# Performance work log

Hardware: AMD Instinct MI355X
Metric: run time of the kernel (lower is better)

## Reference

```python
import jax, jax.numpy as jnp
import numpy as np
from jax import lax

B, C, H, W = 256, 768, 24, 24


def _corner_mask(h, w):
    # corners are never considered peaks in the original nested loops
    m = np.zeros((h, w), dtype=bool)
    m[[0, 0, -1, -1], [0, -1, 0, -1]] = True
    return jnp.asarray(m)


def get_peaks_pool(feat):
    # feat: [B, C, H, W]
    hm = jnp.mean(feat, axis=1)  # [B, H, W]
    # 3x3 local max/min with window clipped at the image border (SAME pad with
    # identity elements), exactly matching the original edge-case loops.
    mx = lax.reduce_window(hm, -jnp.inf, lax.max, (1, 3, 3), (1, 1, 1), 'SAME')
    mn = lax.reduce_window(hm, jnp.inf, lax.min, (1, 3, 3), (1, 1, 1), 'SAME')
    corner = _corner_mask(hm.shape[1], hm.shape[2])
    max_mask = ((hm >= mx) & ~corner).astype(feat.dtype)  # [B, H, W]
    min_mask = ((hm <= mn) & ~corner).astype(feat.dtype)
    # masked mean of feature vectors at peak locations
    f_max = jnp.einsum('bchw,bhw->bc', feat, max_mask) / jnp.sum(max_mask, axis=(1, 2))[:, None]
    f_min = jnp.einsum('bchw,bhw->bc', feat, min_mask) / jnp.sum(min_mask, axis=(1, 2))[:, None]
    f_gap = jnp.mean(feat, axis=(2, 3))  # global average pool
    return jnp.stack([f_max, f_min, f_gap], axis=2)  # [B, C, 3]


def _l2norm(x):
    return x / jnp.linalg.norm(x, axis=-1, keepdims=True)


def _cross_entropy(logits):
    # labels = arange(B): mean of -log_softmax diagonal
    logp = jax.nn.log_softmax(logits, axis=-1)
    return -jnp.mean(jnp.diagonal(logp))


def setup_inputs() -> dict:
    key = jax.random.key(0)
    k1, k2 = jax.random.split(key)
    return {
        'image_features1': jax.random.normal(k1, (B, C, H, W), dtype=jnp.float32),
        'image_features2': jax.random.normal(k2, (B, C, H, W), dtype=jnp.float32),
        'logit_scale': jnp.full((1,), 14.285, dtype=jnp.float32),
    }


def reference(image_features1, image_features2, logit_scale):
    p1 = get_peaks_pool(image_features1)  # [B, C, 3]
    p2 = get_peaks_pool(image_features2)
    e1 = _l2norm(jnp.concatenate([p1[:, :, 0], p1[:, :, 1], p1[:, :, 2]], axis=-1))  # [B, 3C]
    e2 = _l2norm(jnp.concatenate([p2[:, :, 0], p2[:, :, 1], p2[:, :, 2]], axis=-1))
    logits1 = logit_scale.reshape(()) * (e1 @ e2.T)  # [B, B]
    logits2 = logits1.T
    return (_cross_entropy(logits1) + _cross_entropy(logits2)) / 2
```

## Files before the change

kernel.cpp:

```cpp
#include <hip/hip_runtime.h>
#include <math.h>

#define BB   256
#define CC   768
#define HHX  24
#define WWX  24
#define HWX  576
#define EDIM 2304
#define NIMG 2

__global__ void k1_hm(const float* __restrict__ f1, const float* __restrict__ f2,
                      float* __restrict__ hm) {
    int blk = blockIdx.x;
    int img = blk >> 8;
    int b   = blk & 255;
    const float* base = ((img == 0) ? f1 : f2) + (size_t)b * CC * HWX;
    int t = threadIdx.x;
    float acc = 0.f;
    #pragma unroll 8
    for (int c = 0; c < CC; ++c)
        acc += base[(size_t)c * HWX + t];
    hm[(size_t)blk * HWX + t] = acc;
}

__global__ void k2_mask(const float* __restrict__ hm, float* __restrict__ mmax,
                        float* __restrict__ mmin, float* __restrict__ cnt) {
    int blk = blockIdx.x;
    int t = threadIdx.x;
    __shared__ float sh[HWX];
    __shared__ int c0, c1;
    if (t == 0) { c0 = 0; c1 = 0; }
    float v = hm[(size_t)blk * HWX + t];
    sh[t] = v;
    __syncthreads();

    int h = t / WWX, w = t % WWX;
    float mx = -__builtin_inff(), mn = __builtin_inff();
    #pragma unroll
    for (int dh = -1; dh <= 1; ++dh) {
        int hh = h + dh;
        if (hh < 0 || hh >= HHX) continue;
        #pragma unroll
        for (int dw = -1; dw <= 1; ++dw) {
            int ww = w + dw;
            if (ww < 0 || ww >= WWX) continue;
            float u = sh[hh * WWX + ww];
            mx = fmaxf(mx, u);
            mn = fminf(mn, u);
        }
    }
    bool corner = (t == 0) || (t == WWX - 1) || (t == (HHX - 1) * WWX) || (t == HWX - 1);
    bool ismax = (v >= mx) && !corner;
    bool ismin = (v <= mn) && !corner;
    mmax[(size_t)blk * HWX + t] = ismax ? 1.f : 0.f;
    mmin[(size_t)blk * HWX + t] = ismin ? 1.f : 0.f;
    if (ismax) atomicAdd(&c0, 1);
    if (ismin) atomicAdd(&c1, 1);
    __syncthreads();
    if (t == 0) {
        cnt[blk * 2 + 0] = (float)c0;
        cnt[blk * 2 + 1] = (float)c1;
    }
}

__global__ void k3_sums(const float* __restrict__ f1, const float* __restrict__ f2,
                        const float* __restrict__ mmax, const float* __restrict__ mmin,
                        float* __restrict__ sums) {
    int blk = blockIdx.x;
    int img = blk >> 8, b = blk & 255;
    const float* base = ((img == 0) ? f1 : f2) + (size_t)b * CC * HWX;
    int lane = threadIdx.x & 63;
    int wv   = threadIdx.x >> 6;

    float mm[9], mn[9];
    #pragma unroll
    for (int j = 0; j < 9; ++j) {
        mm[j] = mmax[(size_t)blk * HWX + lane + 64 * j];
        mn[j] = mmin[(size_t)blk * HWX + lane + 64 * j];
    }
    float* out = sums + (size_t)blk * EDIM;

    for (int c = wv; c < CC; c += 4) {
        const float* p = base + (size_t)c * HWX;
        float s0 = 0.f, s1 = 0.f, s2 = 0.f;
        #pragma unroll
        for (int j = 0; j < 9; ++j) {
            float v = p[lane + 64 * j];
            s0 += v;
            s1 = fmaf(v, mm[j], s1);
            s2 = fmaf(v, mn[j], s2);
        }
        #pragma unroll
        for (int off = 32; off; off >>= 1) {
            s0 += __shfl_down(s0, off, 64);
            s1 += __shfl_down(s1, off, 64);
            s2 += __shfl_down(s2, off, 64);
        }
        if (lane == 0) {
            out[c]          = s1;
            out[CC + c]     = s2;
            out[2 * CC + c] = s0;
        }
    }
}

__global__ void k4_norm(float* __restrict__ sums, const float* __restrict__ cnt,
                        float* __restrict__ e2t) {
    int blk = blockIdx.x;
    int img = blk >> 8, b = blk & 255;
    int t = threadIdx.x;
    float invmax = 1.f / cnt[blk * 2 + 0];
    float invmin = 1.f / cnt[blk * 2 + 1];
    const float invgap = 1.f / (float)HWX;
    float* e = sums + (size_t)blk * EDIM;

    float val[9];
    float sq = 0.f;
    #pragma unroll
    for (int j = 0; j < 9; ++j) {
        int k = t + 256 * j;
        float d = (k < CC) ? invmax : (k < 2 * CC) ? invmin : invgap;
        float v = e[k] * d;
        val[j] = v;
        sq = fmaf(v, v, sq);
    }
    __shared__ float red[256];
    red[t] = sq;
    __syncthreads();
    for (int s = 128; s; s >>= 1) {
        if (t < s) red[t] += red[t + s];
        __syncthreads();
    }
    float rn = 1.f / sqrtf(red[0]);
    #pragma unroll
    for (int j = 0; j < 9; ++j) {
        int k = t + 256 * j;
        float v = val[j] * rn;
        e[k] = v;
        if (img == 1) e2t[(size_t)k * BB + b] = v;
    }
}

__global__ void k5_logits(const float* __restrict__ e, const float* __restrict__ e2t,
                          const float* __restrict__ scale_p, float* __restrict__ logits) {
    int blk = blockIdx.x;
    int j = threadIdx.x;
    __shared__ float s1[4][EDIM];
    for (int r = 0; r < 4; ++r)
        for (int k = j; k < EDIM; k += 256)
            s1[r][k] = e[(size_t)(4 * blk + r) * EDIM + k];
    __syncthreads();
    float scale = scale_p[0];
    float a0 = 0.f, a1 = 0.f, a2 = 0.f, a3 = 0.f;
    for (int k = 0; k < EDIM; ++k) {
        float bv = e2t[(size_t)k * BB + j];
        a0 = fmaf(s1[0][k], bv, a0);
        a1 = fmaf(s1[1][k], bv, a1);
        a2 = fmaf(s1[2][k], bv, a2);
        a3 = fmaf(s1[3][k], bv, a3);
    }
    logits[(size_t)(4 * blk + 0) * BB + j] = scale * a0;
    logits[(size_t)(4 * blk + 1) * BB + j] = scale * a1;
    logits[(size_t)(4 * blk + 2) * BB + j] = scale * a2;
    logits[(size_t)(4 * blk + 3) * BB + j] = scale * a3;
}

__global__ void k6_loss(const float* __restrict__ logits, float* __restrict__ out) {
    int i = threadIdx.x;
    float rmax = -__builtin_inff(), cmax = -__builtin_inff();
    for (int k = 0; k < BB; ++k) {
        rmax = fmaxf(rmax, logits[(size_t)i * BB + k]);
        cmax = fmaxf(cmax, logits[(size_t)k * BB + i]);
    }
    float rs = 0.f, cs = 0.f;
    for (int k = 0; k < BB; ++k) {
        rs += expf(logits[(size_t)i * BB + k] - rmax);
        cs += expf(logits[(size_t)k * BB + i] - cmax);
    }
    float lser = rmax + logf(rs);
    float lsec = cmax + logf(cs);
    float diag = logits[(size_t)i * BB + i];
    float v = 0.5f * (lser + lsec) - diag;

    __shared__ float red[256];
    red[i] = v;
    __syncthreads();
    for (int s = 128; s; s >>= 1) {
        if (i < s) red[i] += red[i + s];
        __syncthreads();
    }
    if (i == 0) out[0] = red[0] * (1.f / (float)BB);
}

extern "C" void kernel_launch(void* const* d_in, const int* in_sizes, int n_in,
                              void* d_out, int out_size, void* d_ws, size_t ws_size,
                              hipStream_t stream) {
    const float* f1 = (const float*)d_in[0];
    const float* f2 = (const float*)d_in[1];
    const float* scale_p = (const float*)d_in[2];
    float* out = (float*)d_out;

    float* ws = (float*)d_ws;
    const size_t off_hm     = 0;
    const size_t off_mmax   = off_hm     + (size_t)NIMG * BB * HWX;
    const size_t off_mmin   = off_mmax   + (size_t)NIMG * BB * HWX;
    const size_t off_cnt    = off_mmin   + (size_t)NIMG * BB * HWX;
    const size_t off_sums   = off_cnt    + (size_t)NIMG * BB * 2;
    const size_t off_e2t    = off_sums   + (size_t)NIMG * BB * EDIM;
    const size_t off_logits = off_e2t    + (size_t)EDIM * BB;

    float* hm     = ws + off_hm;
    float* mmax   = ws + off_mmax;
    float* mmin   = ws + off_mmin;
    float* cnt    = ws + off_cnt;
    float* sums   = ws + off_sums;
    float* e2t    = ws + off_e2t;
    float* logits = ws + off_logits;

    hipLaunchKernelGGL(k1_hm,    dim3(NIMG * BB), dim3(HWX), 0, stream, f1, f2, hm);
    hipLaunchKernelGGL(k2_mask,  dim3(NIMG * BB), dim3(HWX), 0, stream, hm, mmax, mmin, cnt);
    hipLaunchKernelGGL(k3_sums,  dim3(NIMG * BB), dim3(256), 0, stream, f1, f2, mmax, mmin, sums);
    hipLaunchKernelGGL(k4_norm,  dim3(NIMG * BB), dim3(256), 0, stream, sums, cnt, e2t);
    hipLaunchKernelGGL(k5_logits, dim3(64),       dim3(256), 0, stream, sums, e2t, scale_p, logits);
    hipLaunchKernelGGL(k6_loss,  dim3(1),         dim3(256), 0, stream, logits, out);
}
```

Before: 1.207 ms.

## Vectorize feature reads, fuse mask into sums kernel, parallelize logits and loss

The channel-sum kernel now reads float4 and splits channels across four thread groups with a shared-memory final reduction. The mask computation moves into the weighted-sum kernel, keeping masks in shared memory, and that kernel uses 512 threads with float4 loads. The logits kernel now computes two rows per block and also writes a transposed copy. The single-block loss is split into a parallel row/column log-sum-exp kernel plus a small final reduction. The intent is to raise memory bandwidth on the two full passes over the features and to remove the serial loss loop, at the cost of more kernels and extra workspace.

```diff
diff --git a/kernel.cpp b/kernel.cpp
--- a/kernel.cpp
+++ b/kernel.cpp
@@ -6,6 +6,7 @@
 #define HHX  24
 #define WWX  24
 #define HWX  576
+#define HW4  144
 #define EDIM 2304
 #define NIMG 2
 
@@ -15,81 +16,106 @@
     int img = blk >> 8;
     int b   = blk & 255;
     const float* base = ((img == 0) ? f1 : f2) + (size_t)b * CC * HWX;
+    const float4* base4 = (const float4*)base;
     int t = threadIdx.x;
-    float acc = 0.f;
+    int pos4 = t % HW4;
+    int cg   = t / HW4;
+    float4 acc = make_float4(0.f, 0.f, 0.f, 0.f);
     #pragma unroll 8
-    for (int c = 0; c < CC; ++c)
-        acc += base[(size_t)c * HWX + t];
-    hm[(size_t)blk * HWX + t] = acc;
-}
-
-__global__ void k2_mask(const float* __restrict__ hm, float* __restrict__ mmax,
-                        float* __restrict__ mmin, float* __restrict__ cnt) {
-    int blk = blockIdx.x;
+    for (int c = cg; c < CC; c += 4) {
+        float4 v = base4[(size_t)c * HW4 + pos4];
+        acc.x += v.x; acc.y += v.y; acc.z += v.z; acc.w += v.w;
+    }
+    __shared__ float4 part[HWX];
+    part[t] = acc;
+    __syncthreads();
+    if (t < HW4) {
+        float4 a = part[t], b4 = part[t + HW4], c4 = part[t + 2 * HW4], d4 = part[t + 3 * HW4];
+        float4 s;
+        s.x = a.x + b4.x + c4.x + d4.x;
+        s.y = a.y + b4.y + c4.y + d4.y;
+        s.z = a.z + b4.z + c4.z + d4.z;
+        s.w = a.w + b4.w + c4.w + d4.w;
+        ((float4*)(hm + (size_t)blk * HWX))[t] = s;
+    }
+}
+
+__global__ void k3_sums(const float* __restrict__ f1, const float* __restrict__ f2,
+                        const float* __restrict__ hm, float* __restrict__ cnt,
+                        float* __restrict__ sums) {
+    int blk = blockIdx.x;
+    int img = blk >> 8, b = blk & 255;
+    const float* base = ((img == 0) ? f1 : f2) + (size_t)b * CC * HWX;
     int t = threadIdx.x;
-    __shared__ float sh[HWX];
+    int lane = t & 63;
+    int wv   = t >> 6;
+
+    __shared__ __align__(16) float sh[HWX];
+    __shared__ __align__(16) float smm[HWX];
+    __shared__ __align__(16) float smn[HWX];
     __shared__ int c0, c1;
+
+    sh[t] = hm[(size_t)blk * HWX + t];
+    if (t < HWX - 512) sh[512 + t] = hm[(size_t)blk * HWX + 512 + t];
     if (t == 0) { c0 = 0; c1 = 0; }
-    float v = hm[(size_t)blk * HWX + t];
-    sh[t] = v;
-    __syncthreads();
-
-    int h = t / WWX, w = t % WWX;
-    float mx = -__builtin_inff(), mn = __builtin_inff();
-    #pragma unroll
-    for (int dh = -1; dh <= 1; ++dh) {
-        int hh = h + dh;
-        if (hh < 0 || hh >= HHX) continue;
+    __syncthreads();
+
+    for (int p = t; p < HWX; p += 512) {
+        int h = p / WWX, w = p % WWX;
+        float v = sh[p];
+        float mx = -__builtin_inff(), mn = __builtin_inff();
         #pragma unroll
-        for (int dw = -1; dw <= 1; ++dw) {
-            int ww = w + dw;
-            if (ww < 0 || ww >= WWX) continue;
-            float u = sh[hh * WWX + ww];
-            mx = fmaxf(mx, u);
-            mn = fminf(mn, u);
+        for (int dh = -1; dh <= 1; ++dh) {
+            int hh = h + dh;
+            if (hh < 0 || hh >= HHX) continue;
+            #pragma unroll
+            for (int dw = -1; dw <= 1; ++dw) {
+                int ww = w + dw;
+                if (ww < 0 || ww >= WWX) continue;
+                float u = sh[hh * WWX + ww];
+                mx = fmaxf(mx, u);
+                mn = fminf(mn, u);
+            }
         }
-    }
-    bool corner = (t == 0) || (t == WWX - 1) || (t == (HHX - 1) * WWX) || (t == HWX - 1);
-    bool ismax = (v >= mx) && !corner;
-    bool ismin = (v <= mn) && !corner;
-    mmax[(size_t)blk * HWX + t] = ismax ? 1.f : 0.f;
-    mmin[(size_t)blk * HWX + t] = ismin ? 1.f : 0.f;
-    if (ismax) atomicAdd(&c0, 1);
-    if (ismin) atomicAdd(&c1, 1);
+        bool corner = (p == 0) || (p == WWX - 1) || (p == (HHX - 1) * WWX) || (p == HWX - 1);
+        bool ismax = (v >= mx) && !corner;
+        bool ismin = (v <= mn) && !corner;
+        smm[p] = ismax ? 1.f : 0.f;
+        smn[p] = ismin ? 1.f : 0.f;
+        if (ismax) atomicAdd(&c0, 1);
+        if (ismin) atomicAdd(&c1, 1);
+    }
     __syncthreads();
     if (t == 0) {
         cnt[blk * 2 + 0] = (float)c0;
         cnt[blk * 2 + 1] = (float)c1;
     }
-}
-
-__global__ void k3_sums(const float* __restrict__ f1, const float* __restrict__ f2,
-                        const float* __restrict__ mmax, const float* __restrict__ mmin,
-                        float* __restrict__ sums) {
-    int blk = blockIdx.x;
-    int img = blk >> 8, b = blk & 255;
-    const float* base = ((img == 0) ? f1 : f2) + (size_t)b * CC * HWX;
-    int lane = threadIdx.x & 63;
-    int wv   = threadIdx.x >> 6;
-
-    float mm[9], mn[9];
-    #pragma unroll
-    for (int j = 0; j < 9; ++j) {
-        mm[j] = mmax[(size_t)blk * HWX + lane + 64 * j];
-        mn[j] = mmin[(size_t)blk * HWX + lane + 64 * j];
-    }
+
+    float4 ma0 = ((const float4*)smm)[lane];
+    float4 ma1 = ((const float4*)smm)[64 + lane];
+    float  ma2 = smm[512 + lane];
+    float4 mi0 = ((const float4*)smn)[lane];
+    float4 mi1 = ((const float4*)smn)[64 + lane];
+    float  mi2 = smn[512 + lane];
+
     float* out = sums + (size_t)blk * EDIM;
 
-    for (int c = wv; c < CC; c += 4) {
-        const float* p = base + (size_t)c * HWX;
-        float s0 = 0.f, s1 = 0.f, s2 = 0.f;
-        #pragma unroll
-        for (int j = 0; j < 9; ++j) {
-            float v = p[lane + 64 * j];
-            s0 += v;
-            s1 = fmaf(v, mm[j], s1);
-            s2 = fmaf(v, mn[j], s2);
-        }
+    for (int c = wv; c < CC; c += 8) {
+        const float4* p4 = (const float4*)(base + (size_t)c * HWX);
+        float4 v0 = p4[lane];
+        float4 v1 = p4[64 + lane];
+        float  v2 = (base + (size_t)c * HWX)[512 + lane];
+
+        float s0 = v0.x + v0.y + v0.z + v0.w + v1.x + v1.y + v1.z + v1.w + v2;
+        float s1 = v0.x * ma0.x + v0.y * ma0.y + v0.z * ma0.z + v0.w * ma0.w;
+        s1 = fmaf(v1.x, ma1.x, s1); s1 = fmaf(v1.y, ma1.y, s1);
+        s1 = fmaf(v1.z, ma1.z, s1); s1 = fmaf(v1.w, ma1.w, s1);
+        s1 = fmaf(v2, ma2, s1);
+        float s2 = v0.x * mi0.x + v0.y * mi0.y + v0.z * mi0.z + v0.w * mi0.w;
+        s2 = fmaf(v1.x, mi1.x, s2); s2 = fmaf(v1.y, mi1.y, s2);
+        s2 = fmaf(v1.z, mi1.z, s2); s2 = fmaf(v1.w, mi1.w, s2);
+        s2 = fmaf(v2, mi2, s2);
+
         #pragma unroll
         for (int off = 32; off; off >>= 1) {
             s0 += __shfl_down(s0, off, 64);
@@ -142,46 +168,54 @@
 }
 
 __global__ void k5_logits(const float* __restrict__ e, const float* __restrict__ e2t,
-                          const float* __restrict__ scale_p, float* __restrict__ logits) {
+                          const float* __restrict__ scale_p, float* __restrict__ logits,
+                          float* __restrict__ logitsT) {
     int blk = blockIdx.x;
     int j = threadIdx.x;
-    __shared__ float s1[4][EDIM];
-    for (int r = 0; r < 4; ++r)
+    __shared__ float s1[2][EDIM];
+    for (int r = 0; r < 2; ++r)
         for (int k = j; k < EDIM; k += 256)
-            s1[r][k] = e[(size_t)(4 * blk + r) * EDIM + k];
+            s1[r][k] = e[(size_t)(2 * blk + r) * EDIM + k];
     __syncthreads();
     float scale = scale_p[0];
-    float a0 = 0.f, a1 = 0.f, a2 = 0.f, a3 = 0.f;
-    for (int k = 0; k < EDIM; ++k) {
-        float bv = e2t[(size_t)k * BB + j];
-        a0 = fmaf(s1[0][k], bv, a0);
-        a1 = fmaf(s1[1][k], bv, a1);
-        a2 = fmaf(s1[2][k], bv, a2);
-        a3 = fmaf(s1[3][k], bv, a3);
-    }
-    logits[(size_t)(4 * blk + 0) * BB + j] = scale * a0;
-    logits[(size_t)(4 * blk + 1) * BB + j] = scale * a1;
-    logits[(size_t)(4 * blk + 2) * BB + j] = scale * a2;
-    logits[(size_t)(4 * blk + 3) * BB + j] = scale * a3;
-}
-
-__global__ void k6_loss(const float* __restrict__ logits, float* __restrict__ out) {
+    float a0 = 0.f, a1 = 0.f;
+    for (int k = 0; k < EDIM; k += 4) {
+        float b0 = e2t[(size_t)(k + 0) * BB + j];
+        float b1 = e2t[(size_t)(k + 1) * BB + j];
+        float b2 = e2t[(size_t)(k + 2) * BB + j];
+        float b3 = e2t[(size_t)(k + 3) * BB + j];
+        a0 = fmaf(s1[0][k + 0], b0, a0); a1 = fmaf(s1[1][k + 0], b0, a1);
+        a0 = fmaf(s1[0][k + 1], b1, a0); a1 = fmaf(s1[1][k + 1], b1, a1);
+        a0 = fmaf(s1[0][k + 2], b2, a0); a1 = fmaf(s1[1][k + 2], b2, a1);
+        a0 = fmaf(s1[0][k + 3], b3, a0); a1 = fmaf(s1[1][k + 3], b3, a1);
+    }
+    float r0 = scale * a0, r1 = scale * a1;
+    logits[(size_t)(2 * blk + 0) * BB + j] = r0;
+    logits[(size_t)(2 * blk + 1) * BB + j] = r1;
+    logitsT[(size_t)j * BB + (2 * blk + 0)] = r0;
+    logitsT[(size_t)j * BB + (2 * blk + 1)] = r1;
+}
+
+__global__ void k6_lse(const float* __restrict__ logits, const float* __restrict__ logitsT,
+                       float* __restrict__ lse) {
+    int g = blockIdx.x * 4 + (threadIdx.x >> 6);
+    int lane = threadIdx.x & 63;
+    const float* row = (g < BB) ? (logits + (size_t)g * BB)
+                                : (logitsT + (size_t)(g - BB) * BB);
+    float4 v = ((const float4*)row)[lane];
+    float m = fmaxf(fmaxf(v.x, v.y), fmaxf(v.z, v.w));
+    #pragma unroll
+    for (int off = 32; off; off >>= 1) m = fmaxf(m, __shfl_xor(m, off, 64));
+    float s = expf(v.x - m) + expf(v.y - m) + expf(v.z - m) + expf(v.w - m);
+    #pragma unroll
+    for (int off = 32; off; off >>= 1) s += __shfl_xor(s, off, 64);
+    if (lane == 0) lse[g] = m + logf(s);
+}
+
+__global__ void k7_loss(const float* __restrict__ logits, const float* __restrict__ lse,
+                        float* __restrict__ out) {
     int i = threadIdx.x;
-    float rmax = -__builtin_inff(), cmax = -__builtin_inff();
-    for (int k = 0; k < BB; ++k) {
-        rmax = fmaxf(rmax, logits[(size_t)i * BB + k]);
-        cmax = fmaxf(cmax, logits[(size_t)k * BB + i]);
-    }
-    float rs = 0.f, cs = 0.f;
-    for (int k = 0; k < BB; ++k) {
-        rs += expf(logits[(size_t)i * BB + k] - rmax);
-        cs += expf(logits[(size_t)k * BB + i] - cmax);
-    }
-    float lser = rmax + logf(rs);
-    float lsec = cmax + logf(cs);
-    float diag = logits[(size_t)i * BB + i];
-    float v = 0.5f * (lser + lsec) - diag;
-
+    float v = 0.5f * (lse[i] + lse[BB + i]) - logits[(size_t)i * BB + i];
     __shared__ float red[256];
     red[i] = v;
     __syncthreads();
@@ -201,26 +235,26 @@
     float* out = (float*)d_out;
 
     float* ws = (float*)d_ws;
-    const size_t off_hm     = 0;
-    const size_t off_mmax   = off_hm     + (size_t)NIMG * BB * HWX;
-    const size_t off_mmin   = off_mmax   + (size_t)NIMG * BB * HWX;
-    const size_t off_cnt    = off_mmin   + (size_t)NIMG * BB * HWX;
-    const size_t off_sums   = off_cnt    + (size_t)NIMG * BB * 2;
-    const size_t off_e2t    = off_sums   + (size_t)NIMG * BB * EDIM;
-    const size_t off_logits = off_e2t    + (size_t)EDIM * BB;
-
-    float* hm     = ws + off_hm;
-    float* mmax   = ws + off_mmax;
-    float* mmin   = ws + off_mmin;
-    float* cnt    = ws + off_cnt;
-    float* sums   = ws + off_sums;
-    float* e2t    = ws + off_e2t;
-    float* logits = ws + off_logits;
-
-    hipLaunchKernelGGL(k1_hm,    dim3(NIMG * BB), dim3(HWX), 0, stream, f1, f2, hm);
-    hipLaunchKernelGGL(k2_mask,  dim3(NIMG * BB), dim3(HWX), 0, stream, hm, mmax, mmin, cnt);
-    hipLaunchKernelGGL(k3_sums,  dim3(NIMG * BB), dim3(256), 0, stream, f1, f2, mmax, mmin, sums);
-    hipLaunchKernelGGL(k4_norm,  dim3(NIMG * BB), dim3(256), 0, stream, sums, cnt, e2t);
-    hipLaunchKernelGGL(k5_logits, dim3(64),       dim3(256), 0, stream, sums, e2t, scale_p, logits);
-    hipLaunchKernelGGL(k6_loss,  dim3(1),         dim3(256), 0, stream, logits, out);
-}
+    const size_t off_hm      = 0;
+    const size_t off_cnt     = off_hm      + (size_t)NIMG * BB * HWX;
+    const size_t off_sums    = off_cnt     + (size_t)NIMG * BB * 2;
+    const size_t off_e2t     = off_sums    + (size_t)NIMG * BB * EDIM;
+    const size_t off_logits  = off_e2t     + (size_t)EDIM * BB;
+    const size_t off_logitsT = off_logits  + (size_t)BB * BB;
+    const size_t off_lse     = off_logitsT + (size_t)BB * BB;
+
+    float* hm      = ws + off_hm;
+    float* cnt     = ws + off_cnt;
+    float* sums    = ws + off_sums;
+    float* e2t     = ws + off_e2t;
+    float* logits  = ws + off_logits;
+    float* logitsT = ws + off_logitsT;
+    float* lse     = ws + off_lse;
+
+    hipLaunchKernelGGL(k1_hm,     dim3(NIMG * BB), dim3(HWX), 0, stream, f1, f2, hm);
+    hipLaunchKernelGGL(k3_sums,   dim3(NIMG * BB), dim3(512), 0, stream, f1, f2, hm, cnt, sums);
+    hipLaunchKernelGGL(k4_norm,   dim3(NIMG * BB), dim3(256), 0, stream, sums, cnt, e2t);
+    hipLaunchKernelGGL(k5_logits, dim3(128),       dim3(256), 0, stream, sums, e2t, scale_p, logits, logitsT);
+    hipLaunchKernelGGL(k6_lse,    dim3(128),       dim3(256), 0, stream, logits, logitsT, lse);
+    hipLaunchKernelGGL(k7_loss,   dim3(1),         dim3(256), 0, stream, logits, lse, out);
+}
```

Result: faster. 1.094 ms (-9.4%).
